# Performance work log

Hardware: AMD Instinct MI355X
Metric: run time of the kernel (lower is better)

## Reference

```python
import jax, jax.numpy as jnp
import numpy as np

DECAY = 0.99
LR = 0.01

def setup_inputs() -> dict:
    key = jax.random.key(0)
    ks = jax.random.split(key, 6)
    B, S, D, M = 4, 4096, 1024, 128
    sD = 1.0 / np.sqrt(D)
    sM = 1.0 / np.sqrt(M)
    return {
        "x": jax.random.normal(ks[0], (B, S, D), dtype=jnp.float32),
        "Wk": jax.random.uniform(ks[1], (M, D), jnp.float32, -sD, sD),
        "bk": jnp.zeros((M,), jnp.float32),
        "Wv": jax.random.uniform(ks[2], (M, D), jnp.float32, -sD, sD),
        "bv": jnp.zeros((M,), jnp.float32),
        "Wq": jax.random.uniform(ks[3], (M, D), jnp.float32, -sD, sD),
        "bq": jnp.zeros((M,), jnp.float32),
        "Wo": jax.random.uniform(ks[4], (D, M), jnp.float32, -sM, sM),
        "bo": jnp.zeros((D,), jnp.float32),
    }

def reference(x, Wk, bk, Wv, bv, Wq, bq, Wo, bo):
    B, S, D = x.shape
    M = Wk.shape[0]
    # Precompute all projections in one batched GEMM each: [B,S,M]
    k = jnp.einsum('bsd,md->bsm', x, Wk) + bk
    v = jnp.einsum('bsd,md->bsm', x, Wv) + bv
    q = jnp.einsum('bsd,md->bsm', x, Wq) + bq

    def step(state, kvq):
        k_t, v_t, q_t = kvq  # each [B, M]
        # readout uses the PRE-update state, matching the torch loop order
        out_t = jnp.einsum('bij,bj->bi', state, q_t)          # [B, M]
        state = DECAY * state + LR * jnp.einsum('bi,bj->bij', v_t, k_t)
        return state, out_t

    state0 = jnp.zeros((B, M, M), x.dtype)
    # scan over time: move seq axis to front -> [S, B, M]
    xs = (jnp.swapaxes(k, 0, 1), jnp.swapaxes(v, 0, 1), jnp.swapaxes(q, 0, 1))
    state, outs = jax.lax.scan(step, state0, xs)
    outs = jnp.swapaxes(outs, 0, 1)                            # [B, S, M]
    y = jnp.einsum('bsm,dm->bsd', outs, Wo) + bo               # [B, S, D]
    return (y, state)
```

## Files before the change

### kernel.cpp

```cpp
#include <hip/hip_runtime.h>
#include <math.h>

namespace {
constexpr int kB = 4;
constexpr int kS = 4096;
constexpr int kD = 1024;
constexpr int kM = 128;
constexpr int kC = 64;
constexpr int kNC = kS / kC;
constexpr int kRS = kB * kS;
constexpr float kLR = 0.01f;
constexpr float kLog2d = -0.0144995696f;
}

typedef __bf16 bf16x8 __attribute__((ext_vector_type(8)));
typedef float  f32x4  __attribute__((ext_vector_type(4)));
typedef unsigned short u16;
typedef unsigned int   u32;

__device__ __forceinline__ u16 f2bf(float f) {
  u32 x = __float_as_uint(f);
  u32 r = (x + 0x7fffu + ((x >> 16) & 1u)) >> 16;
  return (u16)r;
}

__device__ __forceinline__ float bf2f(u16 h) {
  return __uint_as_float(((u32)h) << 16);
}

__device__ __forceinline__ void gl_lds16(const void* g, void* l) {
  __builtin_amdgcn_global_load_lds(
      (const __attribute__((address_space(1))) void*)g,
      (__attribute__((address_space(3))) void*)l, 16, 0, 0);
}

__device__ __forceinline__ f32x4 mf(bf16x8 a, bf16x8 b, f32x4 c) {
  return __builtin_amdgcn_mfma_f32_16x16x32_bf16(a, b, c, 0, 0, 0);
}

__global__ __launch_bounds__(256)
void cast_w_kernel(const float* __restrict__ Wk, const float* __restrict__ Wv,
                   const float* __restrict__ Wq, const float* __restrict__ Wo,
                   u16* __restrict__ Wkvq, u16* __restrict__ Woh)
{
  int i = (blockIdx.x * 256 + threadIdx.x) * 4;
  const float* src;
  u16* dst;
  if (i < 393216) {
    src = (i < 131072) ? Wk + i : (i < 262144) ? Wv + (i - 131072) : Wq + (i - 262144);
    dst = Wkvq + i;
  } else {
    src = Wo + (i - 393216);
    dst = Woh + (i - 393216);
  }
  float4 v = *(const float4*)src;
  ushort4 o;
  o.x = f2bf(v.x); o.y = f2bf(v.y); o.z = f2bf(v.z); o.w = f2bf(v.w);
  *(ushort4*)dst = o;
}

__global__ __launch_bounds__(256)
void fused_proj_intra(const float* __restrict__ x, const u16* __restrict__ Wkvq,
                      const float* __restrict__ bk, const float* __restrict__ bv,
                      const float* __restrict__ bq,
                      u16* __restrict__ Qg, u16* __restrict__ O1g,
                      float* __restrict__ SU)
{
  __shared__ __align__(16) u16 L[32768];
  const int c = blockIdx.x, b = blockIdx.y;
  const int R0 = b * kS + c * kC;
  const int tid = threadIdx.x, w = tid >> 6, lane = tid & 63;
  const int fr = lane & 15, qd = lane >> 4;

  f32x4 acc[4][6] = {};
  const int xrow = tid >> 2, xcol = (tid & 3) * 8;
  const float* xp = x + (size_t)(R0 + xrow) * kD + xcol;
  u16* asDst = &L[xrow * 32 + xcol];
  const u16* wp = Wkvq + (size_t)(96 * w + (lane >> 2)) * kD + (lane & 3) * 8;
  u16* bsDst = &L[2048 + (96 * w) * 32];

  float4 xa = *(const float4*)xp;
  float4 xb = *(const float4*)(xp + 4);
  for (int k0 = 0; k0 < kD; k0 += 32) {
    __syncthreads();
#pragma unroll
    for (int i = 0; i < 6; ++i)
      gl_lds16(wp + k0 + (size_t)(i * 16) * kD, bsDst + i * 512);
    u16 xh8[8];
    xh8[0] = f2bf(xa.x); xh8[1] = f2bf(xa.y); xh8[2] = f2bf(xa.z); xh8[3] = f2bf(xa.w);
    xh8[4] = f2bf(xb.x); xh8[5] = f2bf(xb.y); xh8[6] = f2bf(xb.z); xh8[7] = f2bf(xb.w);
    *(uint4*)asDst = *(uint4*)xh8;
    __syncthreads();
    if (k0 + 32 < kD) {
      xa = *(const float4*)(xp + k0 + 32);
      xb = *(const float4*)(xp + k0 + 36);
    }
    bf16x8 av[4], bvv[6];
#pragma unroll
    for (int mi = 0; mi < 4; ++mi)
      av[mi] = *(const bf16x8*)&L[(mi * 16 + fr) * 32 + qd * 8];
#pragma unroll
    for (int nj = 0; nj < 6; ++nj)
      bvv[nj] = *(const bf16x8*)&L[2048 + (96 * w + nj * 16 + fr) * 32 + qd * 8];
#pragma unroll
    for (int mi = 0; mi < 4; ++mi)
#pragma unroll
      for (int nj = 0; nj < 6; ++nj)
        acc[mi][nj] = mf(av[mi], bvv[nj], acc[mi][nj]);
  }
  __syncthreads();

  float dp63[16];
#pragma unroll
  for (int mi = 0; mi < 4; ++mi)
#pragma unroll
    for (int r = 0; r < 4; ++r)
      dp63[mi * 4 + r] = kLR * exp2f((float)(63 - (mi * 16 + qd * 4 + r)) * kLog2d);

#pragma unroll
  for (int nj = 0; nj < 6; ++nj) {
    const int n = 96 * w + nj * 16 + fr;
    const int slab = n >> 7, j = n & 127;
    const float* bp = (slab == 0) ? bk : (slab == 1) ? bv : bq;
    const float bias = bp[j];
#pragma unroll
    for (int mi = 0; mi < 4; ++mi)
#pragma unroll
      for (int r = 0; r < 4; ++r) {
        const int t = mi * 16 + qd * 4 + r;
        const float val = acc[mi][nj][r] + bias;
        const u16 h = f2bf(val);
        if (slab == 0) {
          L[8192 + (j >> 5) * 2048 + t * 32 + (j & 31)] = h;
          L[24576 + (t >> 5) * 4096 + j * 32 + (t & 31)] = f2bf(val * dp63[mi * 4 + r]);
        } else if (slab == 1) {
          L[16384 + (t >> 5) * 4096 + j * 32 + (t & 31)] = h;
        } else {
          L[(j >> 5) * 2048 + t * 32 + (j & 31)] = h;
          Qg[(size_t)(R0 + t) * kM + j] = h;
        }
      }
  }
  __syncthreads();

  const int mP = (w >> 1) * 32, nP = (w & 1) * 32;
  f32x4 p[2][2] = {};
#pragma unroll
  for (int kp = 0; kp < 4; ++kp) {
    bf16x8 a2[2], b2[2];
#pragma unroll
    for (int mi = 0; mi < 2; ++mi)
      a2[mi] = *(const bf16x8*)&L[kp * 2048 + (mP + mi * 16 + fr) * 32 + qd * 8];
#pragma unroll
    for (int ni = 0; ni < 2; ++ni)
      b2[ni] = *(const bf16x8*)&L[8192 + kp * 2048 + (nP + ni * 16 + fr) * 32 + qd * 8];
#pragma unroll
    for (int mi = 0; mi < 2; ++mi)
#pragma unroll
      for (int ni = 0; ni < 2; ++ni)
        p[mi][ni] = mf(a2[mi], b2[ni], p[mi][ni]);
  }
  __syncthreads();

#pragma unroll
  for (int mi = 0; mi < 2; ++mi)
#pragma unroll
    for (int r = 0; r < 4; ++r) {
      const int t = mP + mi * 16 + qd * 4 + r;
#pragma unroll
      for (int ni = 0; ni < 2; ++ni) {
        const int u = nP + ni * 16 + fr;
        float av2 = 0.f;
        if (u < t) av2 = kLR * exp2f((float)(t - 1 - u) * kLog2d) * p[mi][ni][r];
        L[8192 + (u >> 5) * 2048 + t * 32 + (u & 31)] = f2bf(av2);
      }
    }
  __syncthreads();

  const int mO = (w >> 1) * 32, nO = (w & 1) * 64;
  const int mU = (w >> 1) * 64, nU = (w & 1) * 64;
  f32x4 o1[2][4] = {}, uu[4][4] = {};
#pragma unroll
  for (int kp = 0; kp < 2; ++kp) {
    bf16x8 af[2], vb[4], va[4], ub[4];
#pragma unroll
    for (int mi = 0; mi < 2; ++mi)
      af[mi] = *(const bf16x8*)&L[8192 + kp * 2048 + (mO + mi * 16 + fr) * 32 + qd * 8];
#pragma unroll
    for (int ni = 0; ni < 4; ++ni)
      vb[ni] = *(const bf16x8*)&L[16384 + kp * 4096 + (nO + ni * 16 + fr) * 32 + qd * 8];
#pragma unroll
    for (int mi = 0; mi < 4; ++mi)
      va[mi] = *(const bf16x8*)&L[16384 + kp * 4096 + (mU + mi * 16 + fr) * 32 + qd * 8];
#pragma unroll
    for (int ni = 0; ni < 4; ++ni)
      ub[ni] = *(const bf16x8*)&L[24576 + kp * 4096 + (nU + ni * 16 + fr) * 32 + qd * 8];
#pragma unroll
    for (int mi = 0; mi < 2; ++mi)
#pragma unroll
      for (int ni = 0; ni < 4; ++ni)
        o1[mi][ni] = mf(af[mi], vb[ni], o1[mi][ni]);
#pragma unroll
    for (int mi = 0; mi < 4; ++mi)
#pragma unroll
      for (int ni = 0; ni < 4; ++ni)
        uu[mi][ni] = mf(va[mi], ub[ni], uu[mi][ni]);
  }

#pragma unroll
  for (int mi = 0; mi < 2; ++mi)
#pragma unroll
    for (int ni = 0; ni < 4; ++ni)
#pragma unroll
      for (int r = 0; r < 4; ++r) {
        const int t = mO + mi * 16 + qd * 4 + r, i = nO + ni * 16 + fr;
        O1g[(size_t)(R0 + t) * kM + i] = f2bf(o1[mi][ni][r]);
      }
  float* SUc = SU + (size_t)(b * kNC + c) * (kM * kM);
#pragma unroll
  for (int mi = 0; mi < 4; ++mi)
#pragma unroll
    for (int ni = 0; ni < 4; ++ni)
#pragma unroll
      for (int r = 0; r < 4; ++r) {
        const int i = mU + mi * 16 + qd * 4 + r, j = nU + ni * 16 + fr;
        SUc[i * kM + j] = uu[mi][ni][r];
      }
}

__global__ __launch_bounds__(256)
void scan_kernel(const float* __restrict__ SU, u16* __restrict__ Sb16,
                 float* __restrict__ state_out)
{
  const int e = blockIdx.x * 256 + threadIdx.x;
  const int b = e >> 14, ij = e & 16383;
  const float* base = SU + (size_t)b * kNC * 16384 + ij;
  u16* sb = Sb16 + (size_t)b * kNC * 16384 + ij;
  const float dC = exp2f((float)kC * kLog2d);
  float prev = 0.f;
#pragma unroll 8
  for (int c2 = 0; c2 < kNC; ++c2) {
    const float u = base[(size_t)c2 * 16384];
    sb[(size_t)c2 * 16384] = f2bf(prev);
    prev = fmaf(dC, prev, u);
  }
  state_out[e] = prev;
}

__global__ __launch_bounds__(256)
void fused_combine_out(const u16* __restrict__ Qg, const u16* __restrict__ Sb16,
                       const u16* __restrict__ O1g, const u16* __restrict__ Woh,
                       const float* __restrict__ bo, float* __restrict__ y)
{
  __shared__ __align__(16) u16 L[24576];
  const int c = blockIdx.x, b = blockIdx.y;
  const int R0 = b * kS + c * kC;
  const int tid = threadIdx.x, w = tid >> 6, lane = tid & 63;
  const int fr = lane & 15, qd = lane >> 4;
  const size_t cbS = (size_t)(b * kNC + c) * 16384;

  {
    const u16* gq = Qg + (size_t)(R0 + (lane >> 2)) * kM + w * 32 + (lane & 3) * 8;
    u16* lq = &L[w * 2048];
#pragma unroll
    for (int g = 0; g < 4; ++g)
      gl_lds16(gq + (size_t)(g * 16) * kM, lq + g * 512);
    const u16* gs = Sb16 + cbS + (size_t)(lane >> 2) * kM + w * 32 + (lane & 3) * 8;
    u16* ls = &L[8192 + w * 4096];
#pragma unroll
    for (int g = 0; g < 8; ++g)
      gl_lds16(gs + (size_t)(g * 16) * kM, ls + g * 512);
  }

  const int mO = (w >> 1) * 32, nO = (w & 1) * 64;
  u16 o1h[2][4][4];
#pragma unroll
  for (int mi = 0; mi < 2; ++mi)
#pragma unroll
    for (int ni = 0; ni < 4; ++ni)
#pragma unroll
      for (int r = 0; r < 4; ++r)
        o1h[mi][ni][r] =
            O1g[(size_t)(R0 + mO + mi * 16 + qd * 4 + r) * kM + nO + ni * 16 + fr];
  __syncthreads();

  f32x4 o2[2][4] = {};
#pragma unroll
  for (int kp = 0; kp < 4; ++kp) {
    bf16x8 aq[2], bs[4];
#pragma unroll
    for (int mi = 0; mi < 2; ++mi)
      aq[mi] = *(const bf16x8*)&L[kp * 2048 + (mO + mi * 16 + fr) * 32 + qd * 8];
#pragma unroll
    for (int ni = 0; ni < 4; ++ni)
      bs[ni] = *(const bf16x8*)&L[8192 + kp * 4096 + (nO + ni * 16 + fr) * 32 + qd * 8];
#pragma unroll
    for (int mi = 0; mi < 2; ++mi)
#pragma unroll
      for (int ni = 0; ni < 4; ++ni)
        o2[mi][ni] = mf(aq[mi], bs[ni], o2[mi][ni]);
  }
  __syncthreads();

#pragma unroll
  for (int mi = 0; mi < 2; ++mi)
#pragma unroll
    for (int r = 0; r < 4; ++r) {
      const int t = mO + mi * 16 + qd * 4 + r;
      const float dt = exp2f((float)t * kLog2d);
#pragma unroll
      for (int ni = 0; ni < 4; ++ni) {
        const int i = nO + ni * 16 + fr;
        const float ov = fmaf(dt, o2[mi][ni][r], bf2f(o1h[mi][ni][r]));
        L[(i >> 5) * 2048 + t * 32 + (i & 31)] = f2bf(ov);
      }
    }
  __syncthreads();

#pragma unroll 1
  for (int h = 0; h < 2; ++h) {
    const int n0 = w * 256 + h * 128;
    f32x4 fy[4][8] = {};
#pragma unroll
    for (int kp = 0; kp < 4; ++kp) {
      bf16x8 ao[4], bw[8];
#pragma unroll
      for (int mi = 0; mi < 4; ++mi)
        ao[mi] = *(const bf16x8*)&L[kp * 2048 + (mi * 16 + fr) * 32 + qd * 8];
#pragma unroll
      for (int nj = 0; nj < 8; ++nj)
        bw[nj] = *(const bf16x8*)&Woh[(size_t)(n0 + nj * 16 + fr) * kM + kp * 32 + qd * 8];
#pragma unroll
      for (int mi = 0; mi < 4; ++mi)
#pragma unroll
        for (int nj = 0; nj < 8; ++nj)
          fy[mi][nj] = mf(ao[mi], bw[nj], fy[mi][nj]);
    }
#pragma unroll
    for (int nj = 0; nj < 8; ++nj) {
      const int d = n0 + nj * 16 + fr;
      const float bb = bo[d];
#pragma unroll
      for (int mi = 0; mi < 4; ++mi)
#pragma unroll
        for (int r = 0; r < 4; ++r)
          y[(size_t)(R0 + mi * 16 + qd * 4 + r) * kD + d] = fy[mi][nj][r] + bb;
    }
  }
}

extern "C" void kernel_launch(void* const* d_in, const int* in_sizes, int n_in,
                              void* d_out, int out_size, void* d_ws, size_t ws_size,
                              hipStream_t stream) {
  const float* x  = (const float*)d_in[0];
  const float* Wk = (const float*)d_in[1];
  const float* bk = (const float*)d_in[2];
  const float* Wv = (const float*)d_in[3];
  const float* bv = (const float*)d_in[4];
  const float* Wq = (const float*)d_in[5];
  const float* bq = (const float*)d_in[6];
  const float* Wo = (const float*)d_in[7];
  const float* bo = (const float*)d_in[8];

  char* wsp = (char*)d_ws;
  u16* Wkvq = (u16*)wsp;   wsp += (size_t)384 * 1024 * 2;
  u16* Woh  = (u16*)wsp;   wsp += (size_t)1024 * 128 * 2;
  u16* Qg   = (u16*)wsp;   wsp += (size_t)kRS * kM * 2;
  u16* O1g  = (u16*)wsp;   wsp += (size_t)kRS * kM * 2;
  float* SU = (float*)wsp; wsp += (size_t)kB * kNC * 16384 * 4;
  u16* Sb16 = (u16*)wsp;   wsp += (size_t)kB * kNC * 16384 * 2;

  float* y = (float*)d_out;
  float* state_out = y + (size_t)kRS * kD;

  dim3 blk(256);
  cast_w_kernel<<<dim3(512), blk, 0, stream>>>(Wk, Wv, Wq, Wo, Wkvq, Woh);
  fused_proj_intra<<<dim3(kNC, kB), blk, 0, stream>>>(x, Wkvq, bk, bv, bq, Qg, O1g, SU);
  scan_kernel<<<dim3(kB * 16384 / 256), blk, 0, stream>>>(SU, Sb16, state_out);
  fused_combine_out<<<dim3(kNC, kB), blk, 0, stream>>>(Qg, Sb16, O1g, Woh, bo, y);
}
```

Measured before the change: 189.6 us.

## Double the workgroup size, double-buffer the projection GEMM, and use MFMA-fragment LDS layouts

Moves the two fused kernels from 256 to 512 threads (8 waves), which halves the per-wave output tile. The projection GEMM loop is rebuilt with double-buffered LDS stages for both x and weights, so each step needs one barrier instead of two and loads overlap the MFMAs. LDS tiles and the Q workspace are stored in a fragment-ordered layout (fo64x128 etc.) so MFMA operand reads become contiguous 16-byte loads. In exchange, register and LDS pressure rise with double buffering, and half the threads sit idle during the x staging.

```diff
diff --git a/kernel.cpp b/kernel.cpp
--- a/kernel.cpp
+++ b/kernel.cpp
@@ -36,6 +36,23 @@
 
 __device__ __forceinline__ f32x4 mf(bf16x8 a, bf16x8 b, f32x4 c) {
   return __builtin_amdgcn_mfma_f32_16x16x32_bf16(a, b, c, 0, 0, 0);
+}
+
+__device__ __forceinline__ uint4 pack8(float4 a, float4 b) {
+  union { u16 h[8]; uint4 u; } r;
+  r.h[0] = f2bf(a.x); r.h[1] = f2bf(a.y); r.h[2] = f2bf(a.z); r.h[3] = f2bf(a.w);
+  r.h[4] = f2bf(b.x); r.h[5] = f2bf(b.y); r.h[6] = f2bf(b.z); r.h[7] = f2bf(b.w);
+  return r.u;
+}
+
+__device__ __forceinline__ int fo64x128(int r, int c) {
+  return ((r >> 4) * 4 + (c >> 5)) * 1024 + ((c >> 3) & 3) * 256 + (r & 15) * 16 + (c & 7) * 2;
+}
+__device__ __forceinline__ int fo128x64(int r, int c) {
+  return ((r >> 4) * 2 + (c >> 5)) * 1024 + ((c >> 3) & 3) * 256 + (r & 15) * 16 + (c & 7) * 2;
+}
+__device__ __forceinline__ int fo64x64(int r, int c) {
+  return ((r >> 4) * 2 + (c >> 5)) * 1024 + ((c >> 3) & 3) * 256 + (r & 15) * 16 + (c & 7) * 2;
 }
 
 __global__ __launch_bounds__(256)
@@ -59,7 +76,7 @@
   *(ushort4*)dst = o;
 }
 
-__global__ __launch_bounds__(256)
+__global__ __launch_bounds__(512)
 void fused_proj_intra(const float* __restrict__ x, const u16* __restrict__ Wkvq,
                       const float* __restrict__ bk, const float* __restrict__ bv,
                       const float* __restrict__ bq,
@@ -72,43 +89,59 @@
   const int tid = threadIdx.x, w = tid >> 6, lane = tid & 63;
   const int fr = lane & 15, qd = lane >> 4;
 
-  f32x4 acc[4][6] = {};
-  const int xrow = tid >> 2, xcol = (tid & 3) * 8;
-  const float* xp = x + (size_t)(R0 + xrow) * kD + xcol;
-  u16* asDst = &L[xrow * 32 + xcol];
-  const u16* wp = Wkvq + (size_t)(96 * w + (lane >> 2)) * kD + (lane & 3) * 8;
-  u16* bsDst = &L[2048 + (96 * w) * 32];
-
-  float4 xa = *(const float4*)xp;
-  float4 xb = *(const float4*)(xp + 4);
-  for (int k0 = 0; k0 < kD; k0 += 32) {
+  constexpr int As0 = 0, As1 = 4096, Bs0 = 8192, Bs1 = 32768;
+  constexpr int QsB = 0, KsB = 16384, VtB = 32768, KwB = 49152, AtB = 16384;
+
+  f32x4 acc[4][3] = {};
+  const int xrow = tid >> 2, xslot = tid & 3;
+  const float* xp = x;
+  if (tid < 256) xp = x + (size_t)(R0 + xrow) * kD + xslot * 8;
+  const int xoff = (xrow >> 4) * 1024 + xslot * 256 + (xrow & 15) * 16;
+  const u16* wg = Wkvq + (size_t)(48 * w + fr) * kD + qd * 8;
+
+  float4 xa, xb;
+  if (tid < 256) {
+    float4 a0 = *(const float4*)xp;
+    float4 b0 = *(const float4*)(xp + 4);
+    *(uint4*)&L[(As0 + xoff) >> 1] = pack8(a0, b0);
+  }
+#pragma unroll
+  for (int j = 0; j < 3; ++j)
+    gl_lds16(wg + (size_t)j * 16 * kD, &L[(Bs0 + (3 * w + j) * 1024) >> 1]);
+  if (tid < 256) { xa = *(const float4*)(xp + 32); xb = *(const float4*)(xp + 36); }
+  __syncthreads();
+
+#pragma unroll 2
+  for (int i = 0; i < 32; ++i) {
+    const int AsC = (i & 1) ? As1 : As0, BsC = (i & 1) ? Bs1 : Bs0;
+    const int AsN = (i & 1) ? As0 : As1, BsN = (i & 1) ? Bs0 : Bs1;
+    if (i < 31) {
+      const int k1 = (i + 1) * 32;
+#pragma unroll
+      for (int j = 0; j < 3; ++j)
+        gl_lds16(wg + k1 + (size_t)j * 16 * kD, &L[(BsN + (3 * w + j) * 1024) >> 1]);
+      if (tid < 256) {
+        *(uint4*)&L[(AsN + xoff) >> 1] = pack8(xa, xb);
+        if (i < 30) {
+          xa = *(const float4*)(xp + (i + 2) * 32);
+          xb = *(const float4*)(xp + (i + 2) * 32 + 4);
+        }
+      }
+    }
+    bf16x8 av[4], bw3[3];
+#pragma unroll
+    for (int mi = 0; mi < 4; ++mi)
+      av[mi] = *(const bf16x8*)&L[(AsC + mi * 1024 + qd * 256 + fr * 16) >> 1];
+#pragma unroll
+    for (int nj = 0; nj < 3; ++nj)
+      bw3[nj] = *(const bf16x8*)&L[(BsC + (3 * w + nj) * 1024 + qd * 256 + fr * 16) >> 1];
+#pragma unroll
+    for (int mi = 0; mi < 4; ++mi)
+#pragma unroll
+      for (int nj = 0; nj < 3; ++nj)
+        acc[mi][nj] = mf(av[mi], bw3[nj], acc[mi][nj]);
     __syncthreads();
-#pragma unroll
-    for (int i = 0; i < 6; ++i)
-      gl_lds16(wp + k0 + (size_t)(i * 16) * kD, bsDst + i * 512);
-    u16 xh8[8];
-    xh8[0] = f2bf(xa.x); xh8[1] = f2bf(xa.y); xh8[2] = f2bf(xa.z); xh8[3] = f2bf(xa.w);
-    xh8[4] = f2bf(xb.x); xh8[5] = f2bf(xb.y); xh8[6] = f2bf(xb.z); xh8[7] = f2bf(xb.w);
-    *(uint4*)asDst = *(uint4*)xh8;
-    __syncthreads();
-    if (k0 + 32 < kD) {
-      xa = *(const float4*)(xp + k0 + 32);
-      xb = *(const float4*)(xp + k0 + 36);
-    }
-    bf16x8 av[4], bvv[6];
-#pragma unroll
-    for (int mi = 0; mi < 4; ++mi)
-      av[mi] = *(const bf16x8*)&L[(mi * 16 + fr) * 32 + qd * 8];
-#pragma unroll
-    for (int nj = 0; nj < 6; ++nj)
-      bvv[nj] = *(const bf16x8*)&L[2048 + (96 * w + nj * 16 + fr) * 32 + qd * 8];
-#pragma unroll
-    for (int mi = 0; mi < 4; ++mi)
-#pragma unroll
-      for (int nj = 0; nj < 6; ++nj)
-        acc[mi][nj] = mf(av[mi], bvv[nj], acc[mi][nj]);
-  }
-  __syncthreads();
+  }
 
   float dp63[16];
 #pragma unroll
@@ -117,12 +150,14 @@
     for (int r = 0; r < 4; ++r)
       dp63[mi * 4 + r] = kLR * exp2f((float)(63 - (mi * 16 + qd * 4 + r)) * kLog2d);
 
-#pragma unroll
-  for (int nj = 0; nj < 6; ++nj) {
-    const int n = 96 * w + nj * 16 + fr;
-    const int slab = n >> 7, j = n & 127;
+  const size_t qchunk = (size_t)(b * kNC + c) * 8192;
+#pragma unroll
+  for (int nj = 0; nj < 3; ++nj) {
+    const int pn = 3 * w + nj;
+    const int slab = pn >> 3;
+    const int jj = (pn & 7) * 16 + fr;
     const float* bp = (slab == 0) ? bk : (slab == 1) ? bv : bq;
-    const float bias = bp[j];
+    const float bias = bp[jj];
 #pragma unroll
     for (int mi = 0; mi < 4; ++mi)
 #pragma unroll
@@ -131,101 +166,80 @@
         const float val = acc[mi][nj][r] + bias;
         const u16 h = f2bf(val);
         if (slab == 0) {
-          L[8192 + (j >> 5) * 2048 + t * 32 + (j & 31)] = h;
-          L[24576 + (t >> 5) * 4096 + j * 32 + (t & 31)] = f2bf(val * dp63[mi * 4 + r]);
+          L[(KsB + fo64x128(t, jj)) >> 1] = h;
+          L[(KwB + fo128x64(jj, t)) >> 1] = f2bf(val * dp63[mi * 4 + r]);
         } else if (slab == 1) {
-          L[16384 + (t >> 5) * 4096 + j * 32 + (t & 31)] = h;
+          L[(VtB + fo128x64(jj, t)) >> 1] = h;
         } else {
-          L[(j >> 5) * 2048 + t * 32 + (j & 31)] = h;
-          Qg[(size_t)(R0 + t) * kM + j] = h;
+          L[(QsB + fo64x128(t, jj)) >> 1] = h;
+          Qg[qchunk + (fo64x128(t, jj) >> 1)] = h;
         }
       }
   }
   __syncthreads();
 
-  const int mP = (w >> 1) * 32, nP = (w & 1) * 32;
-  f32x4 p[2][2] = {};
-#pragma unroll
-  for (int kp = 0; kp < 4; ++kp) {
-    bf16x8 a2[2], b2[2];
-#pragma unroll
-    for (int mi = 0; mi < 2; ++mi)
-      a2[mi] = *(const bf16x8*)&L[kp * 2048 + (mP + mi * 16 + fr) * 32 + qd * 8];
-#pragma unroll
-    for (int ni = 0; ni < 2; ++ni)
-      b2[ni] = *(const bf16x8*)&L[8192 + kp * 2048 + (nP + ni * 16 + fr) * 32 + qd * 8];
-#pragma unroll
-    for (int mi = 0; mi < 2; ++mi)
-#pragma unroll
-      for (int ni = 0; ni < 2; ++ni)
-        p[mi][ni] = mf(a2[mi], b2[ni], p[mi][ni]);
-  }
-  __syncthreads();
-
-#pragma unroll
-  for (int mi = 0; mi < 2; ++mi)
+  const int tp = w >> 1, up0 = (w & 1) * 2;
+  f32x4 p2[2] = {};
+  {
+    bf16x8 aq[4];
+#pragma unroll
+    for (int kp = 0; kp < 4; ++kp)
+      aq[kp] = *(const bf16x8*)&L[(QsB + (tp * 4 + kp) * 1024 + qd * 256 + fr * 16) >> 1];
+#pragma unroll
+    for (int ui = 0; ui < 2; ++ui)
+#pragma unroll
+      for (int kp = 0; kp < 4; ++kp) {
+        bf16x8 bks = *(const bf16x8*)&L[(KsB + ((up0 + ui) * 4 + kp) * 1024 + qd * 256 + fr * 16) >> 1];
+        p2[ui] = mf(aq[kp], bks, p2[ui]);
+      }
+  }
+  __syncthreads();
+
+#pragma unroll
+  for (int ui = 0; ui < 2; ++ui)
 #pragma unroll
     for (int r = 0; r < 4; ++r) {
-      const int t = mP + mi * 16 + qd * 4 + r;
-#pragma unroll
-      for (int ni = 0; ni < 2; ++ni) {
-        const int u = nP + ni * 16 + fr;
-        float av2 = 0.f;
-        if (u < t) av2 = kLR * exp2f((float)(t - 1 - u) * kLog2d) * p[mi][ni][r];
-        L[8192 + (u >> 5) * 2048 + t * 32 + (u & 31)] = f2bf(av2);
-      }
-    }
-  __syncthreads();
-
-  const int mO = (w >> 1) * 32, nO = (w & 1) * 64;
-  const int mU = (w >> 1) * 64, nU = (w & 1) * 64;
-  f32x4 o1[2][4] = {}, uu[4][4] = {};
-#pragma unroll
-  for (int kp = 0; kp < 2; ++kp) {
-    bf16x8 af[2], vb[4], va[4], ub[4];
-#pragma unroll
-    for (int mi = 0; mi < 2; ++mi)
-      af[mi] = *(const bf16x8*)&L[8192 + kp * 2048 + (mO + mi * 16 + fr) * 32 + qd * 8];
-#pragma unroll
-    for (int ni = 0; ni < 4; ++ni)
-      vb[ni] = *(const bf16x8*)&L[16384 + kp * 4096 + (nO + ni * 16 + fr) * 32 + qd * 8];
-#pragma unroll
-    for (int mi = 0; mi < 4; ++mi)
-      va[mi] = *(const bf16x8*)&L[16384 + kp * 4096 + (mU + mi * 16 + fr) * 32 + qd * 8];
-#pragma unroll
-    for (int ni = 0; ni < 4; ++ni)
-      ub[ni] = *(const bf16x8*)&L[24576 + kp * 4096 + (nU + ni * 16 + fr) * 32 + qd * 8];
-#pragma unroll
-    for (int mi = 0; mi < 2; ++mi)
-#pragma unroll
-      for (int ni = 0; ni < 4; ++ni)
-        o1[mi][ni] = mf(af[mi], vb[ni], o1[mi][ni]);
-#pragma unroll
-    for (int mi = 0; mi < 4; ++mi)
-#pragma unroll
-      for (int ni = 0; ni < 4; ++ni)
-        uu[mi][ni] = mf(va[mi], ub[ni], uu[mi][ni]);
-  }
-
-#pragma unroll
-  for (int mi = 0; mi < 2; ++mi)
-#pragma unroll
-    for (int ni = 0; ni < 4; ++ni)
-#pragma unroll
-      for (int r = 0; r < 4; ++r) {
-        const int t = mO + mi * 16 + qd * 4 + r, i = nO + ni * 16 + fr;
-        O1g[(size_t)(R0 + t) * kM + i] = f2bf(o1[mi][ni][r]);
-      }
+      const int t = tp * 16 + qd * 4 + r;
+      const int u = (up0 + ui) * 16 + fr;
+      float av2 = 0.f;
+      if (u < t) av2 = kLR * exp2f((float)(t - 1 - u) * kLog2d) * p2[ui][r];
+      L[(AtB + fo64x64(t, u)) >> 1] = f2bf(av2);
+    }
+  __syncthreads();
+
+  const int ip0 = (w & 1) * 4;
+  f32x4 o1[4] = {}, uu[8] = {};
+#pragma unroll
+  for (int uc = 0; uc < 2; ++uc) {
+    bf16x8 aA = *(const bf16x8*)&L[(AtB + (tp * 2 + uc) * 1024 + qd * 256 + fr * 16) >> 1];
+    bf16x8 aV = *(const bf16x8*)&L[(VtB + (w * 2 + uc) * 1024 + qd * 256 + fr * 16) >> 1];
+#pragma unroll
+    for (int ni = 0; ni < 4; ++ni) {
+      bf16x8 bV = *(const bf16x8*)&L[(VtB + ((ip0 + ni) * 2 + uc) * 1024 + qd * 256 + fr * 16) >> 1];
+      o1[ni] = mf(aA, bV, o1[ni]);
+    }
+#pragma unroll
+    for (int jp = 0; jp < 8; ++jp) {
+      bf16x8 bK = *(const bf16x8*)&L[(KwB + (jp * 2 + uc) * 1024 + qd * 256 + fr * 16) >> 1];
+      uu[jp] = mf(aV, bK, uu[jp]);
+    }
+  }
+
+#pragma unroll
+  for (int ni = 0; ni < 4; ++ni)
+#pragma unroll
+    for (int r = 0; r < 4; ++r) {
+      const int t = tp * 16 + qd * 4 + r, i = (ip0 + ni) * 16 + fr;
+      O1g[(size_t)(R0 + t) * kM + i] = f2bf(o1[ni][r]);
+    }
   float* SUc = SU + (size_t)(b * kNC + c) * (kM * kM);
 #pragma unroll
-  for (int mi = 0; mi < 4; ++mi)
-#pragma unroll
-    for (int ni = 0; ni < 4; ++ni)
-#pragma unroll
-      for (int r = 0; r < 4; ++r) {
-        const int i = mU + mi * 16 + qd * 4 + r, j = nU + ni * 16 + fr;
-        SUc[i * kM + j] = uu[mi][ni][r];
-      }
+  for (int jp = 0; jp < 8; ++jp)
+#pragma unroll
+    for (int r = 0; r < 4; ++r) {
+      const int i = w * 16 + qd * 4 + r, j = jp * 16 + fr;
+      SUc[i * kM + j] = uu[jp][r];
+    }
 }
 
 __global__ __launch_bounds__(256)
@@ -247,7 +261,7 @@
   state_out[e] = prev;
 }
 
-__global__ __launch_bounds__(256)
+__global__ __launch_bounds__(512)
 void fused_combine_out(const u16* __restrict__ Qg, const u16* __restrict__ Sb16,
                        const u16* __restrict__ O1g, const u16* __restrict__ Woh,
                        const float* __restrict__ bo, float* __restrict__ y)
@@ -257,94 +271,88 @@
   const int R0 = b * kS + c * kC;
   const int tid = threadIdx.x, w = tid >> 6, lane = tid & 63;
   const int fr = lane & 15, qd = lane >> 4;
-  const size_t cbS = (size_t)(b * kNC + c) * 16384;
-
+  constexpr int QsB = 0, SsB = 16384, OutB = 0;
+  const size_t chunk = (size_t)(b * kNC + c);
+
+  const u16* Qgc = Qg + chunk * 8192;
+#pragma unroll
+  for (int g = 0; g < 2; ++g)
+    gl_lds16(Qgc + (2 * w + g) * 512 + lane * 8, &L[(QsB + (2 * w + g) * 1024) >> 1]);
+  const u16* Sbc = Sb16 + chunk * 16384;
+#pragma unroll
+  for (int g = 0; g < 4; ++g) {
+    const int pn = 4 * w + g, ip = pn >> 2, kc = pn & 3;
+    gl_lds16(Sbc + (size_t)(ip * 16 + fr) * kM + kc * 32 + qd * 8,
+             &L[(SsB + pn * 1024) >> 1]);
+  }
+
+  const int tp = w >> 1, ip0 = (w & 1) * 4;
+  u16 o1h[4][4];
+#pragma unroll
+  for (int ni = 0; ni < 4; ++ni)
+#pragma unroll
+    for (int r = 0; r < 4; ++r)
+      o1h[ni][r] =
+          O1g[(size_t)(R0 + tp * 16 + qd * 4 + r) * kM + (ip0 + ni) * 16 + fr];
+  __syncthreads();
+
+  f32x4 o2[4] = {};
   {
-    const u16* gq = Qg + (size_t)(R0 + (lane >> 2)) * kM + w * 32 + (lane & 3) * 8;
-    u16* lq = &L[w * 2048];
-#pragma unroll
-    for (int g = 0; g < 4; ++g)
-      gl_lds16(gq + (size_t)(g * 16) * kM, lq + g * 512);
-    const u16* gs = Sb16 + cbS + (size_t)(lane >> 2) * kM + w * 32 + (lane & 3) * 8;
-    u16* ls = &L[8192 + w * 4096];
-#pragma unroll
-    for (int g = 0; g < 8; ++g)
-      gl_lds16(gs + (size_t)(g * 16) * kM, ls + g * 512);
-  }
-
-  const int mO = (w >> 1) * 32, nO = (w & 1) * 64;
-  u16 o1h[2][4][4];
-#pragma unroll
-  for (int mi = 0; mi < 2; ++mi)
+    bf16x8 aq[4];
+#pragma unroll
+    for (int kp = 0; kp < 4; ++kp)
+      aq[kp] = *(const bf16x8*)&L[(QsB + (tp * 4 + kp) * 1024 + qd * 256 + fr * 16) >> 1];
 #pragma unroll
     for (int ni = 0; ni < 4; ++ni)
 #pragma unroll
-      for (int r = 0; r < 4; ++r)
-        o1h[mi][ni][r] =
-            O1g[(size_t)(R0 + mO + mi * 16 + qd * 4 + r) * kM + nO + ni * 16 + fr];
-  __syncthreads();
-
-  f32x4 o2[2][4] = {};
-#pragma unroll
-  for (int kp = 0; kp < 4; ++kp) {
-    bf16x8 aq[2], bs[4];
-#pragma unroll
-    for (int mi = 0; mi < 2; ++mi)
-      aq[mi] = *(const bf16x8*)&L[kp * 2048 + (mO + mi * 16 + fr) * 32 + qd * 8];
-#pragma unroll
-    for (int ni = 0; ni < 4; ++ni)
-      bs[ni] = *(const bf16x8*)&L[8192 + kp * 4096 + (nO + ni * 16 + fr) * 32 + qd * 8];
-#pragma unroll
-    for (int mi = 0; mi < 2; ++mi)
-#pragma unroll
-      for (int ni = 0; ni < 4; ++ni)
-        o2[mi][ni] = mf(aq[mi], bs[ni], o2[mi][ni]);
-  }
-  __syncthreads();
-
-#pragma unroll
-  for (int mi = 0; mi < 2; ++mi)
-#pragma unroll
-    for (int r = 0; r < 4; ++r) {
-      const int t = mO + mi * 16 + qd * 4 + r;
-      const float dt = exp2f((float)t * kLog2d);
-#pragma unroll
-      for (int ni = 0; ni < 4; ++ni) {
-        const int i = nO + ni * 16 + fr;
-        const float ov = fmaf(dt, o2[mi][ni][r], bf2f(o1h[mi][ni][r]));
-        L[(i >> 5) * 2048 + t * 32 + (i & 31)] = f2bf(ov);
+      for (int kp = 0; kp < 4; ++kp) {
+        bf16x8 bS = *(const bf16x8*)&L[(SsB + ((ip0 + ni) * 4 + kp) * 1024 + qd * 256 + fr * 16) >> 1];
+        o2[ni] = mf(aq[kp], bS, o2[ni]);
       }
-    }
+  }
+  __syncthreads();
+
+#pragma unroll
+  for (int r = 0; r < 4; ++r) {
+    const int t = tp * 16 + qd * 4 + r;
+    const float dt = exp2f((float)t * kLog2d);
+#pragma unroll
+    for (int ni = 0; ni < 4; ++ni) {
+      const int i = (ip0 + ni) * 16 + fr;
+      const float ov = fmaf(dt, o2[ni][r], bf2f(o1h[ni][r]));
+      L[(OutB + fo64x128(t, i)) >> 1] = f2bf(ov);
+    }
+  }
   __syncthreads();
 
 #pragma unroll 1
   for (int h = 0; h < 2; ++h) {
-    const int n0 = w * 256 + h * 128;
-    f32x4 fy[4][8] = {};
+    const int n0 = w * 128 + h * 64;
+    f32x4 fy[4][4] = {};
 #pragma unroll
     for (int kp = 0; kp < 4; ++kp) {
-      bf16x8 ao[4], bw[8];
+      bf16x8 ao[4], bw[4];
 #pragma unroll
       for (int mi = 0; mi < 4; ++mi)
-        ao[mi] = *(const bf16x8*)&L[kp * 2048 + (mi * 16 + fr) * 32 + qd * 8];
-#pragma unroll
-      for (int nj = 0; nj < 8; ++nj)
-        bw[nj] = *(const bf16x8*)&Woh[(size_t)(n0 + nj * 16 + fr) * kM + kp * 32 + qd * 8];
+        ao[mi] = *(const bf16x8*)&L[(OutB + (mi * 4 + kp) * 1024 + qd * 256 + fr * 16) >> 1];
+#pragma unroll
+      for (int dp = 0; dp < 4; ++dp)
+        bw[dp] = *(const bf16x8*)&Woh[(size_t)(n0 + dp * 16 + fr) * kM + kp * 32 + qd * 8];
 #pragma unroll
       for (int mi = 0; mi < 4; ++mi)
 #pragma unroll
-        for (int nj = 0; nj < 8; ++nj)
-          fy[mi][nj] = mf(ao[mi], bw[nj], fy[mi][nj]);
-    }
-#pragma unroll
-    for (int nj = 0; nj < 8; ++nj) {
-      const int d = n0 + nj * 16 + fr;
+        for (int dp = 0; dp < 4; ++dp)
+          fy[mi][dp] = mf(ao[mi], bw[dp], fy[mi][dp]);
+    }
+#pragma unroll
+    for (int dp = 0; dp < 4; ++dp) {
+      const int d = n0 + dp * 16 + fr;
       const float bb = bo[d];
 #pragma unroll
       for (int mi = 0; mi < 4; ++mi)
 #pragma unroll
         for (int r = 0; r < 4; ++r)
-          y[(size_t)(R0 + mi * 16 + qd * 4 + r) * kD + d] = fy[mi][nj][r] + bb;
+          y[(size_t)(R0 + mi * 16 + qd * 4 + r) * kD + d] = fy[mi][dp][r] + bb;
     }
   }
 }
@@ -373,9 +381,8 @@
   float* y = (float*)d_out;
   float* state_out = y + (size_t)kRS * kD;
 
-  dim3 blk(256);
-  cast_w_kernel<<<dim3(512), blk, 0, stream>>>(Wk, Wv, Wq, Wo, Wkvq, Woh);
-  fused_proj_intra<<<dim3(kNC, kB), blk, 0, stream>>>(x, Wkvq, bk, bv, bq, Qg, O1g, SU);
-  scan_kernel<<<dim3(kB * 16384 / 256), blk, 0, stream>>>(SU, Sb16, state_out);
-  fused_combine_out<<<dim3(kNC, kB), blk, 0, stream>>>(Qg, Sb16, O1g, Woh, bo, y);
-}
+  cast_w_kernel<<<dim3(512), dim3(256), 0, stream>>>(Wk, Wv, Wq, Wo, Wkvq, Woh);
+  fused_proj_intra<<<dim3(kNC, kB), dim3(512), 0, stream>>>(x, Wkvq, bk, bv, bq, Qg, O1g, SU);
+  scan_kernel<<<dim3(kB * 16384 / 256), dim3(256), 0, stream>>>(SU, Sb16, state_out);
+  fused_combine_out<<<dim3(kNC, kB), dim3(512), 0, stream>>>(Qg, Sb16, O1g, Woh, bo, y);
+}
```

Result: no change. 186.3 us (-1.8%).
